# Optimization experiments

Hardware: AMD Instinct MI355X
Metric: run time of the kernel (lower is better)

## Reference

```python
import jax, jax.numpy as jnp
import numpy as np

N_NODES = 100000


def gcn_conv(x, edge_index, W, b):
    """PyG-style GCNConv: h = D^-1/2 (A+I) D^-1/2 (x W) + b."""
    n = x.shape[0]
    loop = jnp.arange(n)
    src = jnp.concatenate([edge_index[0], loop])  # [E+N]
    dst = jnp.concatenate([edge_index[1], loop])  # [E+N]
    # degree computed on destination nodes (PyG gcn_norm with self-loops)
    deg = jnp.zeros((n,), x.dtype).at[dst].add(1.0)
    dinv = jnp.where(deg > 0, jax.lax.rsqrt(deg), 0.0)
    norm = dinv[src] * dinv[dst]  # [E+N]
    h = x @ W  # [n, out]
    msg = h[src] * norm[:, None]  # gather + scale
    out = jax.ops.segment_sum(msg, dst, num_segments=n)  # scatter-add
    return out + b


def setup_inputs() -> dict:
    key = jax.random.key(0)
    ks = jax.random.split(key, 8)
    F_in, H, C = 64, 64, 32
    x = jax.random.normal(ks[0], (N_NODES, F_in), dtype=jnp.float32)
    edge_index = jax.random.randint(ks[1], (2, 1200000), 0, N_NODES, dtype=jnp.int64)
    W1 = jax.random.normal(ks[2], (F_in, H), dtype=jnp.float32) / np.sqrt(F_in)
    b1 = jnp.zeros((H,), jnp.float32)
    W2 = jax.random.normal(ks[3], (H, H), dtype=jnp.float32) / np.sqrt(H)
    b2 = jnp.zeros((H,), jnp.float32)
    Wc = jax.random.normal(ks[4], (H, C), dtype=jnp.float32) / np.sqrt(H)
    bc = jnp.zeros((C,), jnp.float32)
    return {"x": x, "edge_index": edge_index, "W1": W1, "b1": b1,
            "W2": W2, "b2": b2, "Wc": Wc, "bc": bc}


def reference(x, edge_index, W1, b1, W2, b2, Wc, bc):
    h = jnp.tanh(gcn_conv(x, edge_index, W1, b1))
    h = jnp.tanh(gcn_conv(h, edge_index, W2, b2))
    out = h @ Wc + bc
    return (out, h)
```

## Files before the change

kernel.cpp:

```cpp
#include <hip/hip_runtime.h>
#include <hip/hip_bf16.h>
#include <stdint.h>

#define CB_SHIFT 11
#define CB_NODES 2048
#define CAP 28672
#define PT 4096

static __device__ inline uint16_t f2bf(float f) {
    union { float f; uint32_t u; } v; v.f = f;
    uint32_t r = v.u + 0x7FFFu + ((v.u >> 16) & 1u);
    return (uint16_t)(r >> 16);
}
static __device__ inline float bflo(uint32_t u) {
    union { uint32_t u; float f; } v; v.u = u << 16; return v.f;
}
static __device__ inline float bfhi(uint32_t u) {
    union { uint32_t u; float f; } v; v.u = u & 0xFFFF0000u; return v.f;
}

__global__ __launch_bounds__(256) void k_init(const uint32_t* __restrict__ e, int E,
                                              int* __restrict__ flag, int* __restrict__ gcur) {
    int t = threadIdx.x;
    if (t < 64) {
        gcur[t] = 0;
        int cnt = E < 1024 ? E : 1024;
        int nz = 0;
        for (int i = t; i < cnt; i += 64) nz |= (e[2 * i + 1] != 0u);
        int any = __any(nz);
        if (t == 0) *flag = any ? 0 : 1;
    }
}

__global__ __launch_bounds__(256) void k_part(const uint32_t* __restrict__ e, int E,
                                              const int* __restrict__ flag,
                                              int* __restrict__ gcur,
                                              uint32_t* __restrict__ parts) {
    __shared__ int sh_hist[64], sh_off[64], sh_base[64], sh_lcur[64];
    __shared__ uint32_t sh_buf[PT];
    __shared__ uint16_t sh_bkt[PT];
    int t = threadIdx.x;
    int tile0 = blockIdx.x * PT;
    int is64 = *flag;
    if (t < 64) sh_hist[t] = 0;
    __syncthreads();

    uint32_t rec[16]; int cb[16];
    for (int j = 0; j < 16; ++j) {
        int idx = tile0 + j * 256 + t;
        cb[j] = -1;
        if (idx < E) {
            uint32_t s = is64 ? e[2 * idx] : e[idx];
            uint32_t d = is64 ? e[2 * (E + idx)] : e[E + idx];
            rec[j] = (s << CB_SHIFT) | (d & (CB_NODES - 1));
            cb[j] = (int)(d >> CB_SHIFT);
            atomicAdd(&sh_hist[cb[j]], 1);
        }
    }
    __syncthreads();
    if (t < 64) {
        int cnt = sh_hist[t];
        int incl = cnt;
        for (int o = 1; o < 64; o <<= 1) {
            int v = __shfl_up(incl, o);
            if (t >= o) incl += v;
        }
        int ex = incl - cnt;
        sh_off[t] = ex;
        sh_lcur[t] = ex;
        sh_base[t] = (cnt > 0) ? atomicAdd(&gcur[t], cnt) : 0;
    }
    __syncthreads();
    for (int j = 0; j < 16; ++j) {
        if (cb[j] >= 0) {
            int slot = atomicAdd(&sh_lcur[cb[j]], 1);
            sh_buf[slot] = rec[j];
            sh_bkt[slot] = (uint16_t)cb[j];
        }
    }
    __syncthreads();
    int total = min(PT, E - tile0);
    for (int i = t; i < total; i += 256) {
        int b = sh_bkt[i];
        int dest = sh_base[b] + (i - sh_off[b]);
        parts[(size_t)b * CAP + dest] = sh_buf[i];
    }
}

__global__ __launch_bounds__(1024) void k_build(const uint32_t* __restrict__ parts,
                                                const int* __restrict__ gcur,
                                                float* __restrict__ dinv,
                                                int* __restrict__ rowbeg,
                                                int* __restrict__ rowend,
                                                uint32_t* __restrict__ col, int N) {
    __shared__ int hist[CB_NODES], cur[CB_NODES], wsum[16];
    int t = threadIdx.x, cb = blockIdx.x;
    int lane = t & 63, w = t >> 6;
    for (int i = t; i < CB_NODES; i += 1024) hist[i] = 0;
    __syncthreads();
    int cnt = gcur[cb];
    const uint32_t* rp = parts + (size_t)cb * CAP;
    for (int i = t; i < cnt; i += 1024) atomicAdd(&hist[rp[i] & (CB_NODES - 1)], 1);
    __syncthreads();
    int h0 = hist[2 * t], h1 = hist[2 * t + 1];
    int s = h0 + h1;
    int incl = s;
    for (int o = 1; o < 64; o <<= 1) {
        int v = __shfl_up(incl, o);
        if (lane >= o) incl += v;
    }
    if (lane == 63) wsum[w] = incl;
    __syncthreads();
    if (t < 16) {
        int v = wsum[t];
        int inc2 = v;
        for (int o = 1; o < 16; o <<= 1) {
            int u = __shfl_up(inc2, o);
            if (t >= o) inc2 += u;
        }
        wsum[t] = inc2 - v;
    }
    __syncthreads();
    int ex = wsum[w] + incl - s;
    int b0 = ex, b1 = ex + h0;
    cur[2 * t] = b0;
    cur[2 * t + 1] = b1;
    int n0 = cb * CB_NODES;
    int base = cb * CAP;
    if (n0 + 2 * t < N) {
        rowbeg[n0 + 2 * t] = base + b0;
        rowend[n0 + 2 * t] = base + b0 + h0;
        dinv[n0 + 2 * t] = rsqrtf((float)(h0 + 1));
    }
    if (n0 + 2 * t + 1 < N) {
        rowbeg[n0 + 2 * t + 1] = base + b1;
        rowend[n0 + 2 * t + 1] = base + b1 + h1;
        dinv[n0 + 2 * t + 1] = rsqrtf((float)(h1 + 1));
    }
    __syncthreads();
    for (int i = t; i < cnt; i += 1024) {
        uint32_t rec = rp[i];
        int pos = atomicAdd(&cur[rec & (CB_NODES - 1)], 1);
        col[base + pos] = rec >> CB_SHIFT;
    }
}

__global__ __launch_bounds__(256) void k_gemm(const float* __restrict__ A,
                                              const float* __restrict__ W,
                                              const float* __restrict__ dinv,
                                              uint16_t* __restrict__ out, int N) {
    __shared__ __align__(16) float xT[64 * 68];
    __shared__ __align__(16) float Wl[64 * 64];
    int t = threadIdx.x;
#pragma unroll
    for (int j = 0; j < 16; ++j) Wl[j * 256 + t] = W[j * 256 + t];
    int n0 = blockIdx.x * 64;
    int nvalid = min(64, N - n0);
#pragma unroll
    for (int j = 0; j < 4; ++j) {
        int flat = j * 256 + t;
        int node = flat >> 4;
        int k4 = (flat & 15) * 4;
        float4 v = make_float4(0.f, 0.f, 0.f, 0.f);
        if (node < nvalid) v = *(const float4*)&A[(size_t)(n0 + node) * 64 + k4];
        xT[(k4 + 0) * 68 + node] = v.x;
        xT[(k4 + 1) * 68 + node] = v.y;
        xT[(k4 + 2) * 68 + node] = v.z;
        xT[(k4 + 3) * 68 + node] = v.w;
    }
    __syncthreads();
    int ng = t >> 4, cg = t & 15;
    float acc[4][4] = {};
#pragma unroll 8
    for (int k = 0; k < 64; ++k) {
        float4 a = *(const float4*)&xT[k * 68 + 4 * ng];
        float4 b = *(const float4*)&Wl[k * 64 + 4 * cg];
        float av[4] = {a.x, a.y, a.z, a.w};
        float bv[4] = {b.x, b.y, b.z, b.w};
#pragma unroll
        for (int i = 0; i < 4; ++i)
#pragma unroll
            for (int j = 0; j < 4; ++j) acc[i][j] = fmaf(av[i], bv[j], acc[i][j]);
    }
#pragma unroll
    for (int i = 0; i < 4; ++i) {
        int ln = 4 * ng + i;
        if (ln < nvalid) {
            int n = n0 + ln;
            float dv = dinv[n];
            ushort4 o;
            o.x = f2bf(acc[i][0] * dv);
            o.y = f2bf(acc[i][1] * dv);
            o.z = f2bf(acc[i][2] * dv);
            o.w = f2bf(acc[i][3] * dv);
            *(ushort4*)&out[(size_t)n * 64 + 4 * cg] = o;
        }
    }
}

__global__ __launch_bounds__(512) void k_agg(const uint16_t* __restrict__ h,
                                             const int* __restrict__ rowbeg,
                                             const int* __restrict__ rowend,
                                             const uint32_t* __restrict__ col,
                                             const float* __restrict__ dinv,
                                             const float* __restrict__ bias,
                                             float* __restrict__ out, int N) {
    int t = threadIdx.x;
    int lane = t & 63, wid = t >> 6;
    int g = lane & 7;
    int sub = lane >> 3;
    const uint4* hp = (const uint4*)h;
    float bv[8];
#pragma unroll
    for (int j = 0; j < 8; ++j) bv[j] = bias[g * 8 + j];
    int wglobal = blockIdx.x * 8 + wid;
    int nwaves = gridDim.x * 8;
    for (int n = wglobal; n < N; n += nwaves) {
        int rs = rowbeg[n], re = rowend[n];
        float acc[8] = {};
        for (int base = rs; base < re; base += 8) {
            int e2 = base + sub;
            if (e2 < re) {
                int src = (int)col[e2];
                uint4 v = hp[(size_t)src * 8 + g];
                acc[0] += bflo(v.x); acc[1] += bfhi(v.x);
                acc[2] += bflo(v.y); acc[3] += bfhi(v.y);
                acc[4] += bflo(v.z); acc[5] += bfhi(v.z);
                acc[6] += bflo(v.w); acc[7] += bfhi(v.w);
            }
        }
#pragma unroll
        for (int m = 8; m < 64; m <<= 1)
#pragma unroll
            for (int j = 0; j < 8; ++j) acc[j] += __shfl_xor(acc[j], m);
        if (sub == 0) {
            float di = dinv[n];
            uint4 v = hp[(size_t)n * 8 + g];
            float hn[8] = {bflo(v.x), bfhi(v.x), bflo(v.y), bfhi(v.y),
                           bflo(v.z), bfhi(v.z), bflo(v.w), bfhi(v.w)};
            __align__(16) float o[8];
#pragma unroll
            for (int j = 0; j < 8; ++j)
                o[j] = tanhf(di * (acc[j] + hn[j]) + bv[j]);
            *(float4*)&out[(size_t)n * 64 + g * 8]     = *(float4*)&o[0];
            *(float4*)&out[(size_t)n * 64 + g * 8 + 4] = *(float4*)&o[4];
        }
    }
}

__global__ __launch_bounds__(256) void k_cls(const float* __restrict__ A,
                                             const float* __restrict__ W,
                                             const float* __restrict__ bc,
                                             float* __restrict__ out, int N) {
    __shared__ __align__(16) float xT[64 * 68];
    __shared__ __align__(16) float Wl[64 * 32];
    int t = threadIdx.x;
#pragma unroll
    for (int j = 0; j < 8; ++j) Wl[j * 256 + t] = W[j * 256 + t];
    int n0 = blockIdx.x * 64;
    int nvalid = min(64, N - n0);
#pragma unroll
    for (int j = 0; j < 4; ++j) {
        int flat = j * 256 + t;
        int node = flat >> 4;
        int k4 = (flat & 15) * 4;
        float4 v = make_float4(0.f, 0.f, 0.f, 0.f);
        if (node < nvalid) v = *(const float4*)&A[(size_t)(n0 + node) * 64 + k4];
        xT[(k4 + 0) * 68 + node] = v.x;
        xT[(k4 + 1) * 68 + node] = v.y;
        xT[(k4 + 2) * 68 + node] = v.z;
        xT[(k4 + 3) * 68 + node] = v.w;
    }
    __syncthreads();
    int ng = t >> 4, cg = t & 15;
    float acc[4][2] = {};
#pragma unroll 8
    for (int k = 0; k < 64; ++k) {
        float4 a = *(const float4*)&xT[k * 68 + 4 * ng];
        float2 b = *(const float2*)&Wl[k * 32 + 2 * cg];
        float av[4] = {a.x, a.y, a.z, a.w};
#pragma unroll
        for (int i = 0; i < 4; ++i) {
            acc[i][0] = fmaf(av[i], b.x, acc[i][0]);
            acc[i][1] = fmaf(av[i], b.y, acc[i][1]);
        }
    }
    float2 bcv = *(const float2*)&bc[2 * cg];
#pragma unroll
    for (int i = 0; i < 4; ++i) {
        int ln = 4 * ng + i;
        if (ln < nvalid) {
            int n = n0 + ln;
            float2 o = make_float2(acc[i][0] + bcv.x, acc[i][1] + bcv.y);
            *(float2*)&out[(size_t)n * 32 + 2 * cg] = o;
        }
    }
}

extern "C" void kernel_launch(void* const* d_in, const int* in_sizes, int n_in,
                              void* d_out, int out_size, void* d_ws, size_t ws_size,
                              hipStream_t stream) {
    const float*    x     = (const float*)d_in[0];
    const uint32_t* edges = (const uint32_t*)d_in[1];
    const float*    W1    = (const float*)d_in[2];
    const float*    b1    = (const float*)d_in[3];
    const float*    W2    = (const float*)d_in[4];
    const float*    b2    = (const float*)d_in[5];
    const float*    Wc    = (const float*)d_in[6];
    const float*    bc    = (const float*)d_in[7];

    const int N   = in_sizes[0] / 64;
    const int E   = in_sizes[1] / 2;
    const int NBC = (N + CB_NODES - 1) >> CB_SHIFT;
    const int NTG = (N + 63) / 64;
    const int NTP = (E + PT - 1) / PT;

    char* w = (char*)d_ws;
    size_t off = 0;
    auto alloc = [&](size_t bytes) {
        void* p = w + off;
        off = (off + bytes + 255) & ~(size_t)255;
        return p;
    };
    int*      flag   = (int*)alloc(4);
    int*      gcur   = (int*)alloc(64 * 4);
    float*    dinv   = (float*)alloc((size_t)N * 4);
    uint32_t* parts  = (uint32_t*)alloc((size_t)NBC * CAP * 4);
    uint32_t* col    = (uint32_t*)alloc((size_t)NBC * CAP * 4);
    int*      rowbeg = (int*)alloc((size_t)N * 4);
    int*      rowend = (int*)alloc((size_t)N * 4);
    uint16_t* bufA   = (uint16_t*)alloc((size_t)N * 64 * 2);

    float* outc = (float*)d_out;
    float* hfin = outc + (size_t)N * 32;

    hipLaunchKernelGGL(k_init, dim3(1), dim3(256), 0, stream, edges, E, flag, gcur);
    hipLaunchKernelGGL(k_part, dim3(NTP), dim3(256), 0, stream, edges, E, flag, gcur, parts);
    hipLaunchKernelGGL(k_build, dim3(NBC), dim3(1024), 0, stream, parts, gcur, dinv, rowbeg, rowend, col, N);

    hipLaunchKernelGGL(k_gemm, dim3(NTG), dim3(256), 0, stream, x, W1, dinv, bufA, N);
    hipLaunchKernelGGL(k_agg, dim3(2048), dim3(512), 0, stream, bufA, rowbeg, rowend, col, dinv, b1, hfin, N);
    hipLaunchKernelGGL(k_gemm, dim3(NTG), dim3(256), 0, stream, hfin, W2, dinv, bufA, N);
    hipLaunchKernelGGL(k_agg, dim3(2048), dim3(512), 0, stream, bufA, rowbeg, rowend, col, dinv, b2, hfin, N);
    hipLaunchKernelGGL(k_cls, dim3(NTG), dim3(256), 0, stream, hfin, Wc, bc, outc, N);
}
```

Before: 285.7 us.

## Map eight nodes per wave in aggregation, use fast tanh, simplify partition ranking

The aggregation kernel now gives each wave eight destination nodes, one per 8-lane group, and loops up to the wave's maximum degree. This replaces the old scheme where a wave handled one node with eight edges in parallel and then did a cross-lane shuffle reduction. Since the grid covers all nodes directly, the grid-stride loop is gone. tanhf is replaced by an exp/rcp approximation, and the partition kernel reuses the atomicAdd return value as each edge's rank instead of running a second atomic pass. The risks are load imbalance from degree divergence inside a wave, small accuracy changes from the fast tanh, and an unused extra pointer parameter.

```diff
diff --git a/kernel.cpp b/kernel.cpp
--- a/kernel.cpp
+++ b/kernel.cpp
@@ -17,6 +17,11 @@
 }
 static __device__ inline float bfhi(uint32_t u) {
     union { uint32_t u; float f; } v; v.u = u & 0xFFFF0000u; return v.f;
+}
+static __device__ inline float tanh_fast(float x) {
+    x = fminf(fmaxf(x, -20.f), 20.f);
+    float e = __expf(2.f * x);
+    return fmaf(-2.f, __builtin_amdgcn_rcpf(e + 1.f), 1.f);
 }
 
 __global__ __launch_bounds__(256) void k_init(const uint32_t* __restrict__ e, int E,
@@ -36,7 +41,7 @@
                                               const int* __restrict__ flag,
                                               int* __restrict__ gcur,
                                               uint32_t* __restrict__ parts) {
-    __shared__ int sh_hist[64], sh_off[64], sh_base[64], sh_lcur[64];
+    __shared__ int sh_hist[64], sh_off[64], sh_base[64];
     __shared__ uint32_t sh_buf[PT];
     __shared__ uint16_t sh_bkt[PT];
     int t = threadIdx.x;
@@ -45,16 +50,18 @@
     if (t < 64) sh_hist[t] = 0;
     __syncthreads();
 
-    uint32_t rec[16]; int cb[16];
+    uint32_t rec[16]; int cb[16], rank[16];
+    const uint2* e2p = (const uint2*)e;
     for (int j = 0; j < 16; ++j) {
         int idx = tile0 + j * 256 + t;
         cb[j] = -1;
         if (idx < E) {
-            uint32_t s = is64 ? e[2 * idx] : e[idx];
-            uint32_t d = is64 ? e[2 * (E + idx)] : e[E + idx];
+            uint32_t s, d;
+            if (is64) { s = e2p[idx].x; d = e2p[E + idx].x; }
+            else      { s = e[idx];     d = e[E + idx]; }
             rec[j] = (s << CB_SHIFT) | (d & (CB_NODES - 1));
             cb[j] = (int)(d >> CB_SHIFT);
-            atomicAdd(&sh_hist[cb[j]], 1);
+            rank[j] = atomicAdd(&sh_hist[cb[j]], 1);
         }
     }
     __syncthreads();
@@ -65,15 +72,13 @@
             int v = __shfl_up(incl, o);
             if (t >= o) incl += v;
         }
-        int ex = incl - cnt;
-        sh_off[t] = ex;
-        sh_lcur[t] = ex;
+        sh_off[t] = incl - cnt;
         sh_base[t] = (cnt > 0) ? atomicAdd(&gcur[t], cnt) : 0;
     }
     __syncthreads();
     for (int j = 0; j < 16; ++j) {
         if (cb[j] >= 0) {
-            int slot = atomicAdd(&sh_lcur[cb[j]], 1);
+            int slot = sh_off[cb[j]] + rank[j];
             sh_buf[slot] = rec[j];
             sh_bkt[slot] = (uint16_t)cb[j];
         }
@@ -204,47 +209,45 @@
                                              const uint32_t* __restrict__ col,
                                              const float* __restrict__ dinv,
                                              const float* __restrict__ bias,
+                                             const float* __restrict__ ,
                                              float* __restrict__ out, int N) {
     int t = threadIdx.x;
     int lane = t & 63, wid = t >> 6;
+    int slot = lane >> 3;
     int g = lane & 7;
-    int sub = lane >> 3;
     const uint4* hp = (const uint4*)h;
     float bv[8];
 #pragma unroll
     for (int j = 0; j < 8; ++j) bv[j] = bias[g * 8 + j];
-    int wglobal = blockIdx.x * 8 + wid;
-    int nwaves = gridDim.x * 8;
-    for (int n = wglobal; n < N; n += nwaves) {
-        int rs = rowbeg[n], re = rowend[n];
-        float acc[8] = {};
-        for (int base = rs; base < re; base += 8) {
-            int e2 = base + sub;
-            if (e2 < re) {
-                int src = (int)col[e2];
-                uint4 v = hp[(size_t)src * 8 + g];
-                acc[0] += bflo(v.x); acc[1] += bfhi(v.x);
-                acc[2] += bflo(v.y); acc[3] += bfhi(v.y);
-                acc[4] += bflo(v.z); acc[5] += bfhi(v.z);
-                acc[6] += bflo(v.w); acc[7] += bfhi(v.w);
-            }
-        }
-#pragma unroll
-        for (int m = 8; m < 64; m <<= 1)
-#pragma unroll
-            for (int j = 0; j < 8; ++j) acc[j] += __shfl_xor(acc[j], m);
-        if (sub == 0) {
-            float di = dinv[n];
-            uint4 v = hp[(size_t)n * 8 + g];
-            float hn[8] = {bflo(v.x), bfhi(v.x), bflo(v.y), bfhi(v.y),
-                           bflo(v.z), bfhi(v.z), bflo(v.w), bfhi(v.w)};
-            __align__(16) float o[8];
-#pragma unroll
-            for (int j = 0; j < 8; ++j)
-                o[j] = tanhf(di * (acc[j] + hn[j]) + bv[j]);
-            *(float4*)&out[(size_t)n * 64 + g * 8]     = *(float4*)&o[0];
-            *(float4*)&out[(size_t)n * 64 + g * 8 + 4] = *(float4*)&o[4];
-        }
+    int n = (blockIdx.x * 8 + wid) * 8 + slot;
+    int rs = 0, deg = 0;
+    if (n < N) { rs = rowbeg[n]; deg = rowend[n] - rs; }
+    int m = deg;
+#pragma unroll
+    for (int o = 1; o < 64; o <<= 1) m = max(m, __shfl_xor(m, o));
+    float acc[8] = {};
+#pragma unroll 2
+    for (int it = 0; it < m; ++it) {
+        if (it < deg) {
+            int src = (int)col[rs + it];
+            uint4 v = hp[(size_t)src * 8 + g];
+            acc[0] += bflo(v.x); acc[1] += bfhi(v.x);
+            acc[2] += bflo(v.y); acc[3] += bfhi(v.y);
+            acc[4] += bflo(v.z); acc[5] += bfhi(v.z);
+            acc[6] += bflo(v.w); acc[7] += bfhi(v.w);
+        }
+    }
+    if (n < N) {
+        float di = dinv[n];
+        uint4 v = hp[(size_t)n * 8 + g];
+        float hn[8] = {bflo(v.x), bfhi(v.x), bflo(v.y), bfhi(v.y),
+                       bflo(v.z), bfhi(v.z), bflo(v.w), bfhi(v.w)};
+        __align__(16) float o[8];
+#pragma unroll
+        for (int j = 0; j < 8; ++j)
+            o[j] = tanh_fast(di * (acc[j] + hn[j]) + bv[j]);
+        *(float4*)&out[(size_t)n * 64 + g * 8]     = *(float4*)&o[0];
+        *(float4*)&out[(size_t)n * 64 + g * 8 + 4] = *(float4*)&o[4];
     }
 }
 
@@ -314,6 +317,7 @@
     const int NBC = (N + CB_NODES - 1) >> CB_SHIFT;
     const int NTG = (N + 63) / 64;
     const int NTP = (E + PT - 1) / PT;
+    const int NAG = (N + 63) / 64;
 
     char* w = (char*)d_ws;
     size_t off = 0;
@@ -339,8 +343,8 @@
     hipLaunchKernelGGL(k_build, dim3(NBC), dim3(1024), 0, stream, parts, gcur, dinv, rowbeg, rowend, col, N);
 
     hipLaunchKernelGGL(k_gemm, dim3(NTG), dim3(256), 0, stream, x, W1, dinv, bufA, N);
-    hipLaunchKernelGGL(k_agg, dim3(2048), dim3(512), 0, stream, bufA, rowbeg, rowend, col, dinv, b1, hfin, N);
+    hipLaunchKernelGGL(k_agg, dim3(NAG), dim3(512), 0, stream, bufA, rowbeg, rowend, col, dinv, b1, (const float*)nullptr, hfin, N);
     hipLaunchKernelGGL(k_gemm, dim3(NTG), dim3(256), 0, stream, hfin, W2, dinv, bufA, N);
-    hipLaunchKernelGGL(k_agg, dim3(2048), dim3(512), 0, stream, bufA, rowbeg, rowend, col, dinv, b2, hfin, N);
+    hipLaunchKernelGGL(k_agg, dim3(NAG), dim3(512), 0, stream, bufA, rowbeg, rowend, col, dinv, b2, (const float*)nullptr, hfin, N);
     hipLaunchKernelGGL(k_cls, dim3(NTG), dim3(256), 0, stream, hfin, Wc, bc, outc, N);
 }
```

After: 257.1 us. -10.0%, faster.
